# Kernel optimization log

Measured on AMD Instinct MI355X. Metric: run time of the kernel, lower is better.

The kernel has to match this reference:

```python
import jax, jax.numpy as jnp
import numpy as np

N_MEL = 80
PRENET = 256
ENC = 512
ARNN = 1024
DRNN = 1024
ATT = 128
NF = 32
K = 31
B, S, T = 16, 256, 400


def _lstm_cell(x, h, c, Wih, Whh, bih, bhh):
    # torch nn.LSTMCell math: gates ordered i, f, g, o
    z = x @ Wih.T + bih + h @ Whh.T + bhh
    i, f, g, o = jnp.split(z, 4, axis=-1)
    c_new = jax.nn.sigmoid(f) * c + jax.nn.sigmoid(i) * jnp.tanh(g)
    h_new = jax.nn.sigmoid(o) * jnp.tanh(c_new)
    return h_new, c_new


def setup_inputs() -> dict:
    key = jax.random.key(0)
    ks = jax.random.split(key, 24)
    g = lambda i, shape: (jax.random.normal(ks[i], shape, jnp.float32) * 0.02)
    inp = {
        'memory': jax.random.normal(ks[0], (B, S, ENC), jnp.float32),
        'decoder_inputs': jax.random.normal(ks[1], (B, N_MEL, T), jnp.float32),
        # prenet (LinearNorm, no bias in tacotron2 prenet)
        'Wpre1': g(2, (PRENET, N_MEL)),
        'Wpre2': g(3, (PRENET, PRENET)),
        # attention LSTMCell: input = prenet + enc = 256 + 512 = 768
        'Wih_a': g(4, (4 * ARNN, PRENET + ENC)),
        'Whh_a': g(5, (4 * ARNN, ARNN)),
        'bih_a': jnp.zeros((4 * ARNN,), jnp.float32),
        'bhh_a': jnp.zeros((4 * ARNN,), jnp.float32),
        # location-sensitive attention
        'Wq': g(6, (ATT, ARNN)),
        'Wm': g(7, (ATT, ENC)),
        'v': g(8, (ATT,)),
        'Wloc_conv': g(9, (NF, 2, K)),
        'Wloc_dense': g(10, (ATT, NF)),
        # decoder LSTMCell: input = att_rnn + enc = 1024 + 512 = 1536
        'Wih_d': g(11, (4 * DRNN, ARNN + ENC)),
        'Whh_d': g(12, (4 * DRNN, DRNN)),
        'bih_d': jnp.zeros((4 * DRNN,), jnp.float32),
        'bhh_d': jnp.zeros((4 * DRNN,), jnp.float32),
        # projections from [decoder_hidden ; context] = 1536
        'Wproj': g(13, (N_MEL, DRNN + ENC)),
        'bproj': jnp.zeros((N_MEL,), jnp.float32),
        'Wgate': g(14, (1, DRNN + ENC)),
        'bgate': jnp.zeros((1,), jnp.float32),
        'memory_lengths': jax.random.randint(ks[15], (B,), S // 2, S + 1),
    }
    return inp


def reference(memory, decoder_inputs, Wpre1, Wpre2, Wih_a, Whh_a, bih_a, bhh_a,
              Wq, Wm, v, Wloc_conv, Wloc_dense, Wih_d, Whh_d, bih_d, bhh_d,
              Wproj, bproj, Wgate, bgate, memory_lengths):
    # pad mask: True where position is beyond the encoder length
    pad_mask = jnp.arange(S)[None, :] >= memory_lengths[:, None]  # [B,S]
    proc_mem = memory @ Wm.T  # [B,S,ATT], memory_layer precomputed once

    # parse_decoder_inputs + go frame: [B,80,T] -> [T,B,80], prepend zeros
    di = jnp.transpose(decoder_inputs, (2, 0, 1))
    di = jnp.concatenate([jnp.zeros((1, B, N_MEL), di.dtype), di], axis=0)
    # prenet (dropout treated as identity for deterministic reference)
    pre = jax.nn.relu(jax.nn.relu(di @ Wpre1.T) @ Wpre2.T)  # [T+1,B,256]
    xs = pre[:-1]  # loop consumes indices 0..T-1

    carry0 = (jnp.zeros((B, ARNN)), jnp.zeros((B, ARNN)),
              jnp.zeros((B, DRNN)), jnp.zeros((B, DRNN)),
              jnp.zeros((B, S)), jnp.zeros((B, S)), jnp.zeros((B, ENC)))

    def step(carry, x):
        ah, ac, dh, dc, aw, awc, ctx = carry
        ah, ac = _lstm_cell(jnp.concatenate([x, ctx], -1), ah, ac,
                            Wih_a, Whh_a, bih_a, bhh_a)
        # location features from [prev_weights ; cum_weights]
        awcat = jnp.stack([aw, awc], axis=1)  # [B,2,S]
        loc = jax.lax.conv_general_dilated(
            awcat, Wloc_conv, (1,), ((K // 2, K // 2),),
            dimension_numbers=('NCH', 'OIH', 'NCH'))  # [B,NF,S]
        proc_att = jnp.einsum('bfs,af->bsa', loc, Wloc_dense)  # [B,S,ATT]
        q = ah @ Wq.T  # [B,ATT]
        e = jnp.tanh(q[:, None, :] + proc_att + proc_mem) @ v  # [B,S]
        e = jnp.where(pad_mask, -1e9, e)
        aw = jax.nn.softmax(e, axis=-1)
        ctx = jnp.einsum('bs,bse->be', aw, memory)  # [B,ENC]
        awc = awc + aw
        dh, dc = _lstm_cell(jnp.concatenate([ah, ctx], -1), dh, dc,
                            Wih_d, Whh_d, bih_d, bhh_d)
        hac = jnp.concatenate([dh, ctx], -1)  # [B,1536]
        mel = hac @ Wproj.T + bproj  # [B,80]
        gate = (hac @ Wgate.T + bgate)[:, 0]  # [B]
        return (ah, ac, dh, dc, aw, awc, ctx), (mel, gate, aw)

    _, (mels, gates, aligns) = jax.lax.scan(step, carry0, xs)
    mel_outputs = jnp.transpose(mels, (1, 2, 0))  # [B,80,T]
    gate_outputs = gates.T  # [B,T]
    alignments = jnp.transpose(aligns, (1, 0, 2))  # [B,T,S]
    return mel_outputs, gate_outputs, alignments
```

## Files before the change

kernel.cpp:

```cpp
#include <hip/hip_runtime.h>

typedef unsigned short ushort_t;
typedef unsigned int uint_t;
typedef float f32x4_t __attribute__((ext_vector_type(4)));
typedef short bf16x8_t __attribute__((ext_vector_type(8)));

#define NBATCH 16
#define SMEM   256
#define TSTEPS 400

#define F_XSB   0u
#define F_PM    819200u
#define F_MMIX  1343488u
#define F_W1T   1675264u
#define F_W2T   1695744u
#define F_AHB   1761280u
#define F_DHB   1777664u
#define F_CTXB  1794048u
#define F_DHF   1802240u
#define F_AWG   1835008u
#define F_FLG   1851392u
#define ZERO_BASE  F_AHB
#define ZERO_COUNT 95616u
#define F_QP    1856896u

#define AHF  0
#define CTXF 64
#define DHFL 192
#define AWF  320
#define PRF  336

#define A_AH    0
#define A_CTX   32768
#define A_XS    49152
#define A_RED   57344
#define A_QWQ   61440
#define A_QH    69632
#define D_AH    0
#define D_CTX   32768
#define D_DH    49152
#define D_COMB  81920
#define M_LOCU  0
#define M_QSM   20480
#define M_VSM   20992
#define M_ESM   21504
#define M_RED   22528
#define M_SMAW  22784
#define M_SMAWC 23808
#define M_MEM   24832
#define M_PART  155904
#define P_DHP   0
#define P_AWP   65536
#define SMEM_BYTES 160000

struct Ptrs {
  const float *memory, *dec_in, *Wpre1, *Wpre2, *Wih_a, *Whh_a, *bih_a, *bhh_a,
              *Wq, *Wm, *v, *Wc, *Wld, *Wih_d, *Whh_d, *bih_d, *bhh_d,
              *Wproj, *bproj, *Wgate, *bgate;
  const int *mlen;
  float *ws;
  float *out;
};

__device__ __forceinline__ float ftanh(float x) {
  float e = __expf(2.f * x);
  return 1.f - 2.f / (e + 1.f);
}
__device__ __forceinline__ float fsig(float x) { return 1.f / (1.f + __expf(-x)); }

__device__ __forceinline__ unsigned f2bfbits(float x) {
  unsigned u = __builtin_bit_cast(unsigned, x);
  return (u + 0x7FFFu + ((u >> 16) & 1u)) >> 16;
}
__device__ __forceinline__ float bf2f(ushort_t u) {
  unsigned v = ((unsigned)u) << 16;
  return __builtin_bit_cast(float, v);
}
__device__ __forceinline__ bf16x8_t packbf8(const float* f) {
  bf16x8_t r;
#pragma unroll
  for (int j = 0; j < 8; ++j) r[j] = (short)f2bfbits(f[j]);
  return r;
}
__device__ __forceinline__ bf16x8_t pack_from_f4(const float* src) {
  const float4* s4 = (const float4*)src;
  float4 lo = s4[0], hi = s4[1];
  float tmp[8] = {lo.x, lo.y, lo.z, lo.w, hi.x, hi.y, hi.z, hi.w};
  return packbf8(tmp);
}
__device__ __forceinline__ bf16x8_t ldbf8(const ushort_t* p) {
  return *(const bf16x8_t*)p;
}
__device__ __forceinline__ unsigned long long ldull_a(const unsigned long long* p) {
  return __hip_atomic_load(p, __ATOMIC_RELAXED, __HIP_MEMORY_SCOPE_AGENT);
}
__device__ __forceinline__ void stull_a(unsigned long long* p, unsigned long long v) {
  __hip_atomic_store(p, v, __ATOMIC_RELAXED, __HIP_MEMORY_SCOPE_AGENT);
}
__device__ __forceinline__ void stf_a(float* p, float v) {
  __hip_atomic_store(p, v, __ATOMIC_RELAXED, __HIP_MEMORY_SCOPE_AGENT);
}
__device__ __forceinline__ float ldf_a(const float* p) {
  return __hip_atomic_load(p, __ATOMIC_RELAXED, __HIP_MEMORY_SCOPE_AGENT);
}
__device__ __forceinline__ void pollge(int* flg, int slot, int thr) {
  while (__hip_atomic_load(flg + slot * 16, __ATOMIC_RELAXED, __HIP_MEMORY_SCOPE_AGENT) < thr)
    __builtin_amdgcn_s_sleep(1);
}
__device__ __forceinline__ void sig(int* flg, int slot, int val) {
  __hip_atomic_store(flg + slot * 16, val, __ATOMIC_RELAXED, __HIP_MEMORY_SCOPE_AGENT);
}
__device__ __forceinline__ void lds_st8(char* smc, int base, int row, int row_sh,
                                        int bytecol, unsigned long long v) {
  *(unsigned long long*)(smc + base + (row << row_sh) + (bytecol ^ ((row & 7) << 4))) = v;
}
__device__ __forceinline__ bf16x8_t lds_bf8(const char* smc, int base, int row,
                                            int row_sh, int bytecol) {
  return *(const bf16x8_t*)(smc + base + (row << row_sh) + (bytecol ^ ((row & 7) << 4)));
}
#define MFMA16(a,b,c) __builtin_amdgcn_mfma_f32_16x16x32_bf16((a),(b),(c),0,0,0)

__global__ __launch_bounds__(256) void k_zero(Ptrs p) {
  unsigned i = blockIdx.x * 256 + threadIdx.x;
  if (i < ZERO_COUNT) p.ws[ZERO_BASE + i] = 0.f;
}

__global__ __launch_bounds__(256) void k_transpose(Ptrs p) {
  int i = blockIdx.x * 256 + threadIdx.x;
  if (i < 20480) {
    int m = i >> 8, c = i & 255;
    p.ws[F_W1T + i] = p.Wpre1[c * 80 + m];
  } else if (i < 20480 + 65536) {
    int j = i - 20480;
    int pp = j >> 8, q = j & 255;
    p.ws[F_W2T + j] = p.Wpre2[q * 256 + pp];
  }
}

__global__ __launch_bounds__(256) void k_prenet(Ptrs p) {
  __shared__ float dil[NBATCH * 80];
  __shared__ float h1[NBATCH * 256];
  const int t = blockIdx.x, tid = threadIdx.x;
  const float* W1T = p.ws + F_W1T;
  const float* W2T = p.ws + F_W2T;

  for (int i = tid; i < NBATCH * 80; i += 256) {
    int b = i / 80, m = i - b * 80;
    dil[i] = (t == 0) ? 0.f : p.dec_in[((size_t)b * 80 + m) * 400 + (t - 1)];
  }
  __syncthreads();

  float acc[NBATCH];
#pragma unroll
  for (int b = 0; b < NBATCH; ++b) acc[b] = 0.f;
  for (int m = 0; m < 80; ++m) {
    float w = W1T[m * 256 + tid];
#pragma unroll
    for (int b = 0; b < NBATCH; ++b) acc[b] = fmaf(dil[b * 80 + m], w, acc[b]);
  }
#pragma unroll
  for (int b = 0; b < NBATCH; ++b) h1[b * 256 + tid] = fmaxf(acc[b], 0.f);
  __syncthreads();

#pragma unroll
  for (int b = 0; b < NBATCH; ++b) acc[b] = 0.f;
  for (int q = 0; q < 256; ++q) {
    float w = W2T[q * 256 + tid];
#pragma unroll
    for (int b = 0; b < NBATCH; ++b) acc[b] = fmaf(h1[b * 256 + q], w, acc[b]);
  }
  ushort_t* xsbU = (ushort_t*)(p.ws + F_XSB);
#pragma unroll
  for (int b = 0; b < NBATCH; ++b)
    xsbU[((size_t)(t * NBATCH + b)) * 256 + tid] = (ushort_t)f2bfbits(fmaxf(acc[b], 0.f));
}

__global__ __launch_bounds__(256) void k_procmem(Ptrs p) {
  __shared__ alignas(16) float msl[16 * 512];
  const int b = blockIdx.x >> 4, s0 = (blockIdx.x & 15) << 4;
  const int tid = threadIdx.x;
  const float4* src = (const float4*)(p.memory + ((size_t)(b * SMEM + s0)) * 512);
  float4* dst = (float4*)msl;
  for (int i = tid; i < 16 * 512 / 4; i += 256) dst[i] = src[i];
  __syncthreads();

  const int a = tid & 127, sg = tid >> 7;
  const float4* wm = (const float4*)(p.Wm + (size_t)a * 512);
  float* pm = p.ws + F_PM;
  float acc[8];
#pragma unroll
  for (int j = 0; j < 8; ++j) acc[j] = 0.f;
  for (int k = 0; k < 128; ++k) {
    float4 w = wm[k];
#pragma unroll
    for (int j = 0; j < 8; ++j) {
      float4 m = ((const float4*)(msl + (size_t)(sg * 8 + j) * 512))[k];
      acc[j] += w.x * m.x + w.y * m.y + w.z * m.z + w.w * m.w;
    }
  }
#pragma unroll
  for (int j = 0; j < 8; ++j)
    pm[((size_t)(b * SMEM + s0 + sg * 8 + j)) * 128 + a] = acc[j];
}

__global__ __launch_bounds__(512) void k_premix(Ptrs p) {
  const int b = blockIdx.x, tid = threadIdx.x;
  float* M = p.ws + F_MMIX;
  for (int i = tid; i < 81 * 256; i += 512) {
    int row = i >> 8, s = i & 255;
    const float* wrow = (row < 80) ? p.Wproj + (size_t)row * 1536 + 1024 : p.Wgate + 1024;
    const float4* w4 = (const float4*)wrow;
    const float4* m4 = (const float4*)(p.memory + ((size_t)(b * 256 + s)) * 512);
    float acc = 0.f;
#pragma unroll 4
    for (int k = 0; k < 128; ++k) {
      float4 w = w4[k], m = m4[k];
      acc += w.x * m.x + w.y * m.y + w.z * m.z + w.w * m.w;
    }
    M[((size_t)b * 81 + row) * 256 + s] = acc;
  }
}

__global__ __launch_bounds__(512, 1) void k_scan(Ptrs p) {
  extern __shared__ char smc[];
  const int bid = blockIdx.x, tid = threadIdx.x;
  const int wid = tid >> 6, lane = tid & 63;
  const int m16 = lane & 15, kq = lane >> 4;

  float* ws = p.ws;
  ushort_t* xsbU  = (ushort_t*)(ws + F_XSB);
  float*    pmF   = ws + F_PM;
  float*    Mx    = ws + F_MMIX;
  unsigned long long* ahb8 = (unsigned long long*)(ws + F_AHB);
  unsigned long long* dhb8 = (unsigned long long*)(ws + F_DHB);
  unsigned long long* ctxb8 = (unsigned long long*)(ws + F_CTXB);
  float*    dhfF  = ws + F_DHF;
  float*    awGF  = ws + F_AWG;
  float*    qpF   = ws + F_QP;
  int*      flg   = (int*)(ws + F_FLG);
  float* out_mel  = p.out;
  float* out_gate = p.out + 512000;
  float* out_al   = p.out + 518400;

  if (bid < 64) {
    const int ls = wid >> 1, half = wid & 1;
    const int strip = (bid << 2) | ls;
    const int gA = m16 & 3, jA = m16 >> 2;
    const int wrowA = gA * 1024 + strip * 4 + jA;
    bf16x8_t wA[28];
#pragma unroll
    for (int c = 0; c < 28; ++c) {
      int k0 = (half * 28 + c) * 32 + kq * 8;
      const float* src = (k0 < 768) ? p.Wih_a + (size_t)wrowA * 768 + k0
                                    : p.Whh_a + (size_t)wrowA * 1024 + (k0 - 768);
      wA[c] = pack_from_f4(src);
    }
    const int nnA = strip * 4 + kq;
    float biasA[4];
#pragma unroll
    for (int r = 0; r < 4; ++r) biasA[r] = p.bih_a[r * 1024 + nnA] + p.bhh_a[r * 1024 + nnA];
    float acState = 0.f;
    float* ared = (float*)(smc + A_RED);
    float* qwq  = (float*)(smc + A_QWQ);
    float* qh   = (float*)(smc + A_QH);
    for (int i = tid; i < 2048; i += 512) {
      int a = i >> 4, c = i & 15;
      qwq[i] = p.Wq[(size_t)a * 1024 + bid * 16 + c];
    }
    __syncthreads();

    for (int t = 0; t < TSTEPS; ++t) {
      const int pc = t & 1, pp = (t + 1) & 1;
      if (tid < 64) pollge(flg, AHF + tid, t);
      else if (tid >= 96 && tid < 224) pollge(flg, DHFL + (tid - 96), t - 1);
      __syncthreads();
      {
        const unsigned long long* ag = ahb8 + (size_t)pp * 4096;
        const unsigned long long* xg = (const unsigned long long*)xsbU + (size_t)t * 1024;
        unsigned long long tA[8], tX[2];
#pragma unroll
        for (int i = 0; i < 8; ++i) tA[i] = ldull_a(ag + tid + i * 512);
#pragma unroll
        for (int i = 0; i < 2; ++i) tX[i] = xg[tid + i * 512];
#pragma unroll
        for (int i = 0; i < 8; ++i) { int u = tid + i * 512; lds_st8(smc, A_AH, u >> 8, 11, (u & 255) * 8, tA[i]); }
#pragma unroll
        for (int i = 0; i < 2; ++i) { int u = tid + i * 512; lds_st8(smc, A_XS, u >> 6, 9, (u & 63) * 8, tX[i]); }
      }
      __syncthreads();
      f32x4_t a0 = {0,0,0,0}, a1 = {0,0,0,0};
      if (half == 0) {
#pragma unroll
        for (int c = 0; c < 8; ++c) {
          bf16x8_t bf = lds_bf8(smc, A_XS, m16, 9, c * 64 + kq * 16);
          if (c & 1) a1 = MFMA16(wA[c], bf, a1); else a0 = MFMA16(wA[c], bf, a0);
        }
#pragma unroll
        for (int c = 24; c < 28; ++c) {
          bf16x8_t bf = lds_bf8(smc, A_AH, m16, 11, (c - 24) * 64 + kq * 16);
          if (c & 1) a1 = MFMA16(wA[c], bf, a1); else a0 = MFMA16(wA[c], bf, a0);
        }
      } else {
#pragma unroll
        for (int c = 0; c < 28; ++c) {
          bf16x8_t bf = lds_bf8(smc, A_AH, m16, 11, (4 + c) * 64 + kq * 16);
          if (c & 1) a1 = MFMA16(wA[c], bf, a1); else a0 = MFMA16(wA[c], bf, a0);
        }
#pragma unroll
        for (int r = 0; r < 4; ++r) ared[((ls * 64 + lane) << 2) + r] = a0[r] + a1[r];
      }
      if (tid < 32) pollge(flg, CTXF + tid, t);
      __syncthreads();
      {
        const unsigned long long* cg = ctxb8 + (size_t)pp * 2048;
        unsigned long long tC[4];
#pragma unroll
        for (int i = 0; i < 4; ++i) tC[i] = ldull_a(cg + tid + i * 512);
#pragma unroll
        for (int i = 0; i < 4; ++i) { int u = tid + i * 512; lds_st8(smc, A_CTX, u >> 7, 10, (u & 127) * 8, tC[i]); }
      }
      __syncthreads();
      if (half == 0) {
#pragma unroll
        for (int c = 8; c < 24; ++c) {
          bf16x8_t bf = lds_bf8(smc, A_CTX, m16, 10, (c - 8) * 64 + kq * 16);
          if (c & 1) a1 = MFMA16(wA[c], bf, a1); else a0 = MFMA16(wA[c], bf, a0);
        }
        float z[4];
#pragma unroll
        for (int r = 0; r < 4; ++r)
          z[r] = a0[r] + a1[r] + ared[((ls * 64 + lane) << 2) + r] + biasA[r];
        float cn = fsig(z[1]) * acState + fsig(z[0]) * ftanh(z[2]);
        acState = cn;
        float h = fsig(z[3]) * ftanh(cn);
        qh[(m16 << 4) + ls * 4 + kq] = h;
        unsigned hb = f2bfbits(h);
        unsigned b0 = __shfl(hb, m16);
        unsigned b1 = __shfl(hb, m16 + 16);
        unsigned b2 = __shfl(hb, m16 + 32);
        unsigned b3 = __shfl(hb, m16 + 48);
        if (kq == 0) {
          unsigned long long u = (unsigned long long)(b0 | (b1 << 16))
                               | ((unsigned long long)(b2 | (b3 << 16)) << 32);
          stull_a(ahb8 + ((size_t)(pc * 16 + m16)) * 256 + strip, u);
        }
      }
      __syncthreads();
      {
        int a = tid & 127, bg = tid >> 7;
        const float* wrow = qwq + a * 16;
        float s0 = 0.f, s1 = 0.f, s2 = 0.f, s3 = 0.f;
#pragma unroll
        for (int c = 0; c < 16; ++c) {
          float wv = wrow[c];
          s0 = fmaf(wv, qh[((bg * 4 + 0) << 4) + c], s0);
          s1 = fmaf(wv, qh[((bg * 4 + 1) << 4) + c], s1);
          s2 = fmaf(wv, qh[((bg * 4 + 2) << 4) + c], s2);
          s3 = fmaf(wv, qh[((bg * 4 + 3) << 4) + c], s3);
        }
        float* qps = qpF + (size_t)pc * 131072 + bid * 2048 + a;
        stf_a(qps + (size_t)(bg * 4 + 0) * 128, s0);
        stf_a(qps + (size_t)(bg * 4 + 1) * 128, s1);
        stf_a(qps + (size_t)(bg * 4 + 2) * 128, s2);
        stf_a(qps + (size_t)(bg * 4 + 3) * 128, s3);
      }
      __syncthreads();
      if (tid == 0) sig(flg, AHF + bid, t + 1);
    }
  } else if (bid < 192) {
    const int ls = wid >> 2, qt = wid & 3;
    const int strip = ((bid - 64) << 1) | ls;
    const int gD = m16 & 3, jD = m16 >> 2;
    const int wrowD = gD * 1024 + strip * 4 + jD;
    bf16x8_t wD[20];
#pragma unroll
    for (int c = 0; c < 20; ++c) {
      int k0 = (qt * 20 + c) * 32 + kq * 8;
      const float* src = (k0 < 1536) ? p.Wih_d + (size_t)wrowD * 1536 + k0
                                     : p.Whh_d + (size_t)wrowD * 1024 + (k0 - 1536);
      wD[c] = pack_from_f4(src);
    }
    const int nnD = strip * 4 + kq;
    float biasD[4];
#pragma unroll
    for (int r = 0; r < 4; ++r) biasD[r] = p.bih_d[r * 1024 + nnD] + p.bhh_d[r * 1024 + nnD];
    float dcState = 0.f;
    float* comb = (float*)(smc + D_COMB);
    __syncthreads();

    for (int t = 1; t <= TSTEPS; ++t) {
      const int pc = t & 1, pw = (t + 1) & 1;
      if (tid < 64) pollge(flg, AHF + tid, t);
      else if (tid >= 96 && tid < 224) pollge(flg, DHFL + (tid - 96), t - 1);
      else if (tid >= 224 && tid < 232) pollge(flg, PRF + (tid - 224), t - 2);
      __syncthreads();
      {
        const unsigned long long* ag = ahb8 + (size_t)pw * 4096;
        const unsigned long long* dg = dhb8 + (size_t)pc * 4096;
        unsigned long long tA[8], tD[8];
#pragma unroll
        for (int i = 0; i < 8; ++i) tA[i] = ldull_a(ag + tid + i * 512);
#pragma unroll
        for (int i = 0; i < 8; ++i) tD[i] = ldull_a(dg + tid + i * 512);
#pragma unroll
        for (int i = 0; i < 8; ++i) { int u = tid + i * 512; lds_st8(smc, D_AH, u >> 8, 11, (u & 255) * 8, tA[i]); }
#pragma unroll
        for (int i = 0; i < 8; ++i) { int u = tid + i * 512; lds_st8(smc, D_DH, u >> 8, 11, (u & 255) * 8, tD[i]); }
      }
      if (tid >= 64 && tid < 96) pollge(flg, CTXF + (tid - 64), t);
      __syncthreads();
      {
        const unsigned long long* cg = ctxb8 + (size_t)pw * 2048;
        unsigned long long tC[4];
#pragma unroll
        for (int i = 0; i < 4; ++i) tC[i] = ldull_a(cg + tid + i * 512);
#pragma unroll
        for (int i = 0; i < 4; ++i) { int u = tid + i * 512; lds_st8(smc, D_CTX, u >> 7, 10, (u & 127) * 8, tC[i]); }
      }
      __syncthreads();

      f32x4_t a0 = {0,0,0,0}, a1 = {0,0,0,0};
#define DFRAG_AH(ch)  lds_bf8(smc, D_AH,  m16, 11, (ch) * 64 + kq * 16)
#define DFRAG_CTX(ch) lds_bf8(smc, D_CTX, m16, 10, (ch) * 64 + kq * 16)
#define DFRAG_DH(ch)  lds_bf8(smc, D_DH,  m16, 11, (ch) * 64 + kq * 16)
#define DMFMA(BF) { bf16x8_t bf = (BF); \
        if (c & 1) a1 = MFMA16(wD[c], bf, a1); else a0 = MFMA16(wD[c], bf, a0); }
      if (qt == 0) {
#pragma unroll
        for (int c = 0; c < 20; ++c) DMFMA(DFRAG_AH(c))
      } else if (qt == 1) {
#pragma unroll
        for (int c = 0; c < 20; ++c) { if (c < 12) DMFMA(DFRAG_AH(20 + c)) else DMFMA(DFRAG_CTX(c - 12)) }
      } else if (qt == 2) {
#pragma unroll
        for (int c = 0; c < 20; ++c) { if (c < 8) DMFMA(DFRAG_CTX(8 + c)) else DMFMA(DFRAG_DH(c - 8)) }
      } else {
#pragma unroll
        for (int c = 0; c < 20; ++c) DMFMA(DFRAG_DH(12 + c))
      }
#undef DMFMA
      if (qt != 0) {
#pragma unroll
        for (int r = 0; r < 4; ++r)
          comb[(((ls * 3 + qt - 1) * 64 + lane) << 2) + r] = a0[r] + a1[r];
      }
      __syncthreads();
      if (qt == 0) {
        float z[4];
#pragma unroll
        for (int r = 0; r < 4; ++r) {
          z[r] = a0[r] + a1[r] + biasD[r];
#pragma unroll
          for (int j = 0; j < 3; ++j) z[r] += comb[(((ls * 3 + j) * 64 + lane) << 2) + r];
        }
        float cn = fsig(z[1]) * dcState + fsig(z[0]) * ftanh(z[2]);
        dcState = cn;
        float h = fsig(z[3]) * ftanh(cn);
        stf_a(dhfF + (size_t)pw * 16384 + m16 * 1024 + nnD, h);
        unsigned hb = f2bfbits(h);
        unsigned b0 = __shfl(hb, m16);
        unsigned b1 = __shfl(hb, m16 + 16);
        unsigned b2 = __shfl(hb, m16 + 32);
        unsigned b3 = __shfl(hb, m16 + 48);
        if (kq == 0) {
          unsigned long long u = (unsigned long long)(b0 | (b1 << 16))
                               | ((unsigned long long)(b2 | (b3 << 16)) << 32);
          stull_a(dhb8 + ((size_t)(pw * 16 + m16)) * 256 + strip, u);
        }
      }
      __syncthreads();
      if (tid == 0) sig(flg, DHFL + (bid - 64), t);
    }
  } else if (bid < 224) {
    const int cbid = bid - 192;
    const int b = cbid >> 1, h2 = cbid & 1;
    const int mlenb = p.mlen[b];
    ushort_t* locu = (ushort_t*)(smc + M_LOCU);
    float* qsm   = (float*)(smc + M_QSM);
    float* vsm   = (float*)(smc + M_VSM);
    float* esm   = (float*)(smc + M_ESM);
    float* red   = (float*)(smc + M_RED);
    float* smaw  = (float*)(smc + M_SMAW);
    float* smawc = (float*)(smc + M_SMAWC);
    ushort_t* memu2 = (ushort_t*)(smc + M_MEM);
    float* part  = (float*)(smc + M_PART);
    float* qred  = part;

    bf16x8_t wLd[8];
#pragma unroll
    for (int at = 0; at < 8; ++at)
      wLd[at] = pack_from_f4(p.Wld + ((size_t)(at * 16 + m16)) * 32 + kq * 8);
    bf16x8_t wC[2][2];
#pragma unroll
    for (int ft = 0; ft < 2; ++ft)
#pragma unroll
      for (int ck = 0; ck < 2; ++ck) {
        float tmp[8];
#pragma unroll
        for (int jj = 0; jj < 8; ++jj) {
          int k2 = ck * 32 + kq * 8 + jj;
          float vv = 0.f;
          if (k2 < 62) { int ch = (k2 < 31) ? 0 : 1; int k = k2 - 31 * ch;
            vv = p.Wc[((size_t)(ft * 16 + m16) * 2 + ch) * 31 + k]; }
          tmp[jj] = vv;
        }
        wC[ft][ck] = packbf8(tmp);
      }
    uint_t pmreg[2][8][2];
#pragma unroll
    for (int u = 0; u < 2; ++u) {
      int sloc = (wid * 2 + u) * 16 + m16;
#pragma unroll
      for (int at = 0; at < 8; ++at)
#pragma unroll
        for (int rp = 0; rp < 2; ++rp) {
          const float* src = pmF + ((size_t)(b * 256 + sloc)) * 128 + at * 16 + kq * 4 + rp * 2;
          pmreg[u][at][rp] = f2bfbits(src[0]) | (f2bfbits(src[1]) << 16);
        }
    }
    for (int i = tid; i < 16384; i += 512) {
      int s = i >> 6, c4 = i & 63;
      float4 m = *(const float4*)(p.memory + ((size_t)(b * 256 + s)) * 512 + h2 * 256 + c4 * 4);
      ushort_t* dst = memu2 + s * 256 + c4 * 4;
      dst[0] = (ushort_t)f2bfbits(m.x);
      dst[1] = (ushort_t)f2bfbits(m.y);
      dst[2] = (ushort_t)f2bfbits(m.z);
      dst[3] = (ushort_t)f2bfbits(m.w);
    }
    if (tid < 128) vsm[tid] = p.v[tid];
    if (tid < 256) { smaw[tid] = 0.f; smawc[tid] = 0.f; }
    __syncthreads();

    for (int t = 0; t < TSTEPS; ++t) {
      const int pc = t & 1;
#pragma unroll
      for (int u = 0; u < 4; ++u) {
        int task = wid * 4 + u;
        int stile = task >> 1, ft = task & 1;
        int scol = stile * 16 + m16;
        f32x4_t acc = {0,0,0,0};
#pragma unroll
        for (int ck = 0; ck < 2; ++ck) {
          float tmp[8];
#pragma unroll
          for (int jj = 0; jj < 8; ++jj) {
            int k2 = ck * 32 + kq * 8 + jj;
            float vv = 0.f;
            if (k2 < 62) {
              int ch = (k2 < 31) ? 0 : 1; int k = k2 - 31 * ch;
              int sp = scol + k - 15;
              if (sp >= 0 && sp < 256) vv = (ch ? smawc : smaw)[sp];
            }
            tmp[jj] = vv;
          }
          acc = MFMA16(wC[ft][ck], packbf8(tmp), acc);
        }
#pragma unroll
        for (int r = 0; r < 4; ++r)
          locu[scol * 40 + ft * 16 + kq * 4 + r] = (ushort_t)f2bfbits(acc[r]);
      }
      if (tid < 64) pollge(flg, AHF + tid, t + 1);
      else if (tid < 192) pollge(flg, DHFL + (tid - 64), t - 1);
      else if (tid < 200) pollge(flg, PRF + (tid - 192), t - 3);
      __syncthreads();
      {
        int a = tid & 127, g = tid >> 7;
        const float* qps = qpF + (size_t)(t & 1) * 131072 + b * 128 + a;
        float s = 0.f;
#pragma unroll
        for (int k = 0; k < 16; ++k)
          s += ldf_a(qps + (size_t)(g * 16 + k) * 2048);
        qred[g * 128 + a] = s;
      }
      __syncthreads();
      if (tid < 128) qsm[tid] = qred[tid] + qred[128 + tid] + qred[256 + tid] + qred[384 + tid];
      __syncthreads();
#pragma unroll
      for (int u = 0; u < 2; ++u) {
        int sloc = (wid * 2 + u) * 16 + m16;
        bf16x8_t Bfrag = ldbf8(locu + sloc * 40 + kq * 8);
        float eacc = 0.f;
#pragma unroll
        for (int at = 0; at < 8; ++at) {
          f32x4_t C = {0,0,0,0};
          C = MFMA16(wLd[at], Bfrag, C);
#pragma unroll
          for (int r = 0; r < 4; ++r) {
            int a = at * 16 + kq * 4 + r;
            uint_t pw_ = pmreg[u][at][r >> 1];
            float pmv = bf2f((ushort_t)((r & 1) ? (pw_ >> 16) : (pw_ & 0xFFFF)));
            eacc = fmaf(vsm[a], ftanh(C[r] + qsm[a] + pmv), eacc);
          }
        }
        eacc += __shfl_xor(eacc, 16);
        eacc += __shfl_xor(eacc, 32);
        if (sloc >= mlenb) eacc = -1.0e9f;
        if (kq == 0) esm[sloc] = eacc;
      }
      __syncthreads();
      float ev = 0.f;
      if (tid < 256) {
        ev = esm[tid];
        float mv = ev;
        for (int o = 32; o; o >>= 1) mv = fmaxf(mv, __shfl_xor(mv, o));
        if (lane == 0) red[wid] = mv;
      }
      __syncthreads();
      float gmax = fmaxf(fmaxf(red[0], red[1]), fmaxf(red[2], red[3]));
      float pv = 0.f;
      if (tid < 256) {
        pv = __expf(ev - gmax);
        float sv = pv;
        for (int o = 32; o; o >>= 1) sv += __shfl_xor(sv, o);
        if (lane == 0) red[8 + wid] = sv;
      }
      __syncthreads();
      float gsum = red[8] + red[9] + red[10] + red[11];
      float awv = 0.f;
      if (tid < 256) {
        awv = pv / gsum;
        smaw[tid] = awv;
        smawc[tid] += awv;
        if (h2 == 0) stf_a(awGF + (size_t)(t & 3) * 4096 + b * 256 + tid, awv);
      }
      __syncthreads();
      {
        const int c = tid & 127, sg = tid >> 7;
        const uint_t* mrow = (const uint_t*)memu2;
        float c0 = 0.f, c1 = 0.f;
#pragma unroll 8
        for (int si = 0; si < 64; ++si) {
          int s = sg * 64 + si;
          uint_t mm = mrow[s * 128 + c];
          float av = smaw[s];
          c0 = fmaf(bf2f((ushort_t)(mm & 0xFFFF)), av, c0);
          c1 = fmaf(bf2f((ushort_t)(mm >> 16)), av, c1);
        }
        part[sg * 256 + c * 2] = c0;
        part[sg * 256 + c * 2 + 1] = c1;
      }
      __syncthreads();
      if (tid < 64) {
        unsigned pk[4];
#pragma unroll
        for (int j = 0; j < 4; ++j) {
          int col = tid * 4 + j;
          float v = part[col] + part[256 + col] + part[512 + col] + part[768 + col];
          pk[j] = f2bfbits(v);
        }
        unsigned long long u = (unsigned long long)(pk[0] | (pk[1] << 16))
                             | ((unsigned long long)(pk[2] | (pk[3] << 16)) << 32);
        stull_a(ctxb8 + ((size_t)(pc * 16 + b)) * 128 + h2 * 64 + tid, u);
      }
      __syncthreads();
      if (tid == 0) {
        sig(flg, CTXF + cbid, t + 1);
        if (h2 == 0) sig(flg, AWF + b, t + 1);
      }
      if (h2 == 0 && tid < 256) out_al[((size_t)b * 400 + t) * 256 + tid] = awv;
    }
  } else if (bid < 232) {
    const int wv = (bid - 224) * 8 + wid;
    int rows[2] = {wv * 2, wv * 2 + 1};
    float wdh[2][16], mreg[2][16][4], biasr[2];
#pragma unroll
    for (int rr = 0; rr < 2; ++rr) {
      int row = rows[rr];
      biasr[rr] = 0.f;
#pragma unroll
      for (int j = 0; j < 16; ++j) wdh[rr][j] = 0.f;
#pragma unroll
      for (int b2 = 0; b2 < 16; ++b2)
#pragma unroll
        for (int j = 0; j < 4; ++j) mreg[rr][b2][j] = 0.f;
      if (row <= 80) {
        const float* wsrc = (row < 80) ? p.Wproj + (size_t)row * 1536 : p.Wgate;
#pragma unroll
        for (int j = 0; j < 16; ++j) wdh[rr][j] = wsrc[lane + 64 * j];
        biasr[rr] = (row < 80) ? p.bproj[row] : p.bgate[0];
#pragma unroll
        for (int b2 = 0; b2 < 16; ++b2)
#pragma unroll
          for (int j = 0; j < 4; ++j)
            mreg[rr][b2][j] = Mx[((size_t)b2 * 81 + row) * 256 + lane + 64 * j];
      }
    }
    float* dhp = (float*)(smc + P_DHP);
    float* awp = (float*)(smc + P_AWP);
    __syncthreads();
    for (int t = 1; t <= TSTEPS; ++t) {
      const int pw = (t + 1) & 1;
      if (tid < 128) pollge(flg, DHFL + tid, t);
      else if (tid < 144) pollge(flg, AWF + tid - 128, t);
      __syncthreads();
      {
        const unsigned long long* ag = (const unsigned long long*)(awGF + (size_t)((t - 1) & 3) * 4096);
        const unsigned long long* dg = (const unsigned long long*)(dhfF + (size_t)pw * 16384);
        unsigned long long tw[4], td[16];
#pragma unroll
        for (int i = 0; i < 4; ++i) tw[i] = ldull_a(ag + tid + i * 512);
#pragma unroll
        for (int i = 0; i < 16; ++i) td[i] = ldull_a(dg + tid + i * 512);
#pragma unroll
        for (int i = 0; i < 4; ++i) ((unsigned long long*)awp)[tid + i * 512] = tw[i];
#pragma unroll
        for (int i = 0; i < 16; ++i) ((unsigned long long*)dhp)[tid + i * 512] = td[i];
      }
      __syncthreads();
      if (wv <= 40) {
        for (int b2 = 0; b2 < 16; ++b2) {
          float h[16];
#pragma unroll
          for (int j = 0; j < 16; ++j) h[j] = dhp[b2 * 1024 + lane + 64 * j];
#pragma unroll
          for (int rr = 0; rr < 2; ++rr) {
            if (rows[rr] > 80) continue;
            float d = 0.f;
#pragma unroll
            for (int j = 0; j < 16; ++j) d = fmaf(wdh[rr][j], h[j], d);
#pragma unroll
            for (int j = 0; j < 4; ++j) d = fmaf(mreg[rr][b2][j], awp[b2 * 256 + lane + 64 * j], d);
            for (int o = 32; o; o >>= 1) d += __shfl_xor(d, o);
            if (lane == 0) {
              d += biasr[rr];
              if (rows[rr] < 80) out_mel[((size_t)b2 * 80 + rows[rr]) * 400 + (t - 1)] = d;
              else out_gate[(size_t)b2 * 400 + (t - 1)] = d;
            }
          }
        }
      }
      __syncthreads();
      if (tid == 0) sig(flg, PRF + (bid - 224), t);
    }
  }
}

extern "C" void kernel_launch(void* const* d_in, const int* in_sizes, int n_in,
                              void* d_out, int out_size, void* d_ws, size_t ws_size,
                              hipStream_t stream) {
  (void)in_sizes; (void)n_in; (void)out_size; (void)ws_size;
  Ptrs p;
  p.memory = (const float*)d_in[0];
  p.dec_in = (const float*)d_in[1];
  p.Wpre1  = (const float*)d_in[2];
  p.Wpre2  = (const float*)d_in[3];
  p.Wih_a  = (const float*)d_in[4];
  p.Whh_a  = (const float*)d_in[5];
  p.bih_a  = (const float*)d_in[6];
  p.bhh_a  = (const float*)d_in[7];
  p.Wq     = (const float*)d_in[8];
  p.Wm     = (const float*)d_in[9];
  p.v      = (const float*)d_in[10];
  p.Wc     = (const float*)d_in[11];
  p.Wld    = (const float*)d_in[12];
  p.Wih_d  = (const float*)d_in[13];
  p.Whh_d  = (const float*)d_in[14];
  p.bih_d  = (const float*)d_in[15];
  p.bhh_d  = (const float*)d_in[16];
  p.Wproj  = (const float*)d_in[17];
  p.bproj  = (const float*)d_in[18];
  p.Wgate  = (const float*)d_in[19];
  p.bgate  = (const float*)d_in[20];
  p.mlen   = (const int*)d_in[21];
  p.ws  = (float*)d_ws;
  p.out = (float*)d_out;

  static bool attr_done = false;
  if (!attr_done) {
    hipFuncSetAttribute((const void*)k_scan,
                        hipFuncAttributeMaxDynamicSharedMemorySize, SMEM_BYTES);
    attr_done = true;
  }

  hipLaunchKernelGGL(k_zero,      dim3((ZERO_COUNT + 255) / 256), dim3(256), 0, stream, p);
  hipLaunchKernelGGL(k_transpose, dim3(336), dim3(256), 0, stream, p);
  hipLaunchKernelGGL(k_prenet,    dim3(400), dim3(256), 0, stream, p);
  hipLaunchKernelGGL(k_procmem,   dim3(256), dim3(256), 0, stream, p);
  hipLaunchKernelGGL(k_premix,    dim3(16),  dim3(512), 0, stream, p);
  hipLaunchKernelGGL(k_scan,      dim3(232), dim3(512), SMEM_BYTES, stream, p);
}
```

Baseline: 8.205 ms.

## Rebalance attention-LSTM K split, read ctx directly from global, defer DH polls

The attention-LSTM weight columns are redistributed so both half-waves do their h/x MFMAs before waiting on context. Context fragments are then loaded straight from global with atomic loads instead of being staged through LDS, which removes a sync and an LDS copy. The polls on the decoder-hidden flags move from the top of the step to just before the ah write-back in the attention blocks, and to before the ctx write-back in the attention-context blocks. This shortens the critical path across the cross-block pipeline, at the cost of more scattered global loads and a changed ordering of the write-after-read guards.

```diff
diff --git a/kernel.cpp b/kernel.cpp
--- a/kernel.cpp
+++ b/kernel.cpp
@@ -31,7 +31,6 @@
 #define PRF  336
 
 #define A_AH    0
-#define A_CTX   32768
 #define A_XS    49152
 #define A_RED   57344
 #define A_QWQ   61440
@@ -94,6 +93,13 @@
 __device__ __forceinline__ unsigned long long ldull_a(const unsigned long long* p) {
   return __hip_atomic_load(p, __ATOMIC_RELAXED, __HIP_MEMORY_SCOPE_AGENT);
 }
+struct ull2_t { unsigned long long x, y; };
+__device__ __forceinline__ bf16x8_t ldbf8_a(const ushort_t* q) {
+  ull2_t v;
+  v.x = __hip_atomic_load((const unsigned long long*)q, __ATOMIC_RELAXED, __HIP_MEMORY_SCOPE_AGENT);
+  v.y = __hip_atomic_load(((const unsigned long long*)q) + 1, __ATOMIC_RELAXED, __HIP_MEMORY_SCOPE_AGENT);
+  return __builtin_bit_cast(bf16x8_t, v);
+}
 __device__ __forceinline__ void stull_a(unsigned long long* p, unsigned long long v) {
   __hip_atomic_store(p, v, __ATOMIC_RELAXED, __HIP_MEMORY_SCOPE_AGENT);
 }
@@ -250,10 +256,16 @@
     bf16x8_t wA[28];
 #pragma unroll
     for (int c = 0; c < 28; ++c) {
-      int k0 = (half * 28 + c) * 32 + kq * 8;
-      const float* src = (k0 < 768) ? p.Wih_a + (size_t)wrowA * 768 + k0
-                                    : p.Whh_a + (size_t)wrowA * 1024 + (k0 - 768);
-      wA[c] = pack_from_f4(src);
+      int k0; const float* base;
+      if (half == 0) {
+        if (c < 8)       { k0 = c * 32;              base = p.Wih_a + (size_t)wrowA * 768; }
+        else if (c < 20) { k0 = (c - 8) * 32;        base = p.Whh_a + (size_t)wrowA * 1024; }
+        else             { k0 = 256 + (c - 20) * 32; base = p.Wih_a + (size_t)wrowA * 768; }
+      } else {
+        if (c < 20)      { k0 = (12 + c) * 32;       base = p.Whh_a + (size_t)wrowA * 1024; }
+        else             { k0 = 256 + (c - 12) * 32; base = p.Wih_a + (size_t)wrowA * 768; }
+      }
+      wA[c] = pack_from_f4(base + k0 + kq * 8);
     }
     const int nnA = strip * 4 + kq;
     float biasA[4];
@@ -272,7 +284,6 @@
     for (int t = 0; t < TSTEPS; ++t) {
       const int pc = t & 1, pp = (t + 1) & 1;
       if (tid < 64) pollge(flg, AHF + tid, t);
-      else if (tid >= 96 && tid < 224) pollge(flg, DHFL + (tid - 96), t - 1);
       __syncthreads();
       {
         const unsigned long long* ag = ahb8 + (size_t)pp * 4096;
@@ -296,36 +307,35 @@
           if (c & 1) a1 = MFMA16(wA[c], bf, a1); else a0 = MFMA16(wA[c], bf, a0);
         }
 #pragma unroll
-        for (int c = 24; c < 28; ++c) {
-          bf16x8_t bf = lds_bf8(smc, A_AH, m16, 11, (c - 24) * 64 + kq * 16);
+        for (int c = 8; c < 20; ++c) {
+          bf16x8_t bf = lds_bf8(smc, A_AH, m16, 11, (c - 8) * 64 + kq * 16);
           if (c & 1) a1 = MFMA16(wA[c], bf, a1); else a0 = MFMA16(wA[c], bf, a0);
         }
       } else {
 #pragma unroll
-        for (int c = 0; c < 28; ++c) {
-          bf16x8_t bf = lds_bf8(smc, A_AH, m16, 11, (4 + c) * 64 + kq * 16);
+        for (int c = 0; c < 20; ++c) {
+          bf16x8_t bf = lds_bf8(smc, A_AH, m16, 11, (12 + c) * 64 + kq * 16);
           if (c & 1) a1 = MFMA16(wA[c], bf, a1); else a0 = MFMA16(wA[c], bf, a0);
         }
+      }
+      if (tid < 32) pollge(flg, CTXF + tid, t);
+      __syncthreads();
+      {
+        const ushort_t* cbase = (const ushort_t*)(ctxb8 + (size_t)pp * 2048) + m16 * 512;
+#pragma unroll
+        for (int c = 20; c < 28; ++c) {
+          int cc = (half == 0) ? (c - 20) : (c - 12);
+          bf16x8_t bf = ldbf8_a(cbase + cc * 32 + kq * 8);
+          if (c & 1) a1 = MFMA16(wA[c], bf, a1); else a0 = MFMA16(wA[c], bf, a0);
+        }
+      }
+      if (half == 1) {
 #pragma unroll
         for (int r = 0; r < 4; ++r) ared[((ls * 64 + lane) << 2) + r] = a0[r] + a1[r];
       }
-      if (tid < 32) pollge(flg, CTXF + tid, t);
-      __syncthreads();
-      {
-        const unsigned long long* cg = ctxb8 + (size_t)pp * 2048;
-        unsigned long long tC[4];
-#pragma unroll
-        for (int i = 0; i < 4; ++i) tC[i] = ldull_a(cg + tid + i * 512);
-#pragma unroll
-        for (int i = 0; i < 4; ++i) { int u = tid + i * 512; lds_st8(smc, A_CTX, u >> 7, 10, (u & 127) * 8, tC[i]); }
-      }
-      __syncthreads();
+      __syncthreads();
+      unsigned long long ahb_u = 0ull;
       if (half == 0) {
-#pragma unroll
-        for (int c = 8; c < 24; ++c) {
-          bf16x8_t bf = lds_bf8(smc, A_CTX, m16, 10, (c - 8) * 64 + kq * 16);
-          if (c & 1) a1 = MFMA16(wA[c], bf, a1); else a0 = MFMA16(wA[c], bf, a0);
-        }
         float z[4];
 #pragma unroll
         for (int r = 0; r < 4; ++r)
@@ -339,13 +349,14 @@
         unsigned b1 = __shfl(hb, m16 + 16);
         unsigned b2 = __shfl(hb, m16 + 32);
         unsigned b3 = __shfl(hb, m16 + 48);
-        if (kq == 0) {
-          unsigned long long u = (unsigned long long)(b0 | (b1 << 16))
-                               | ((unsigned long long)(b2 | (b3 << 16)) << 32);
-          stull_a(ahb8 + ((size_t)(pc * 16 + m16)) * 256 + strip, u);
-        }
-      }
-      __syncthreads();
+        if (kq == 0)
+          ahb_u = (unsigned long long)(b0 | (b1 << 16))
+                | ((unsigned long long)(b2 | (b3 << 16)) << 32);
+      }
+      if (tid < 128) pollge(flg, DHFL + tid, t - 1);
+      __syncthreads();
+      if (half == 0 && kq == 0)
+        stull_a(ahb8 + ((size_t)(pc * 16 + m16)) * 256 + strip, ahb_u);
       {
         int a = tid & 127, bg = tid >> 7;
         const float* wrow = qwq + a * 16;
@@ -560,8 +571,7 @@
           locu[scol * 40 + ft * 16 + kq * 4 + r] = (ushort_t)f2bfbits(acc[r]);
       }
       if (tid < 64) pollge(flg, AHF + tid, t + 1);
-      else if (tid < 192) pollge(flg, DHFL + (tid - 64), t - 1);
-      else if (tid < 200) pollge(flg, PRF + (tid - 192), t - 3);
+      else if (tid < 72) pollge(flg, PRF + (tid - 64), t - 3);
       __syncthreads();
       {
         int a = tid & 127, g = tid >> 7;
@@ -639,6 +649,7 @@
         part[sg * 256 + c * 2] = c0;
         part[sg * 256 + c * 2 + 1] = c1;
       }
+      if (tid < 128) pollge(flg, DHFL + tid, t - 1);
       __syncthreads();
       if (tid < 64) {
         unsigned pk[4];
```

Result: slower. 9.498 ms (+15.8%).
